# Performance work log

Hardware: AMD Instinct MI355X
Metric: run time of the kernel (lower is better)

Reference implementation:

```python
import jax, jax.numpy as jnp
import numpy as np

HIDDEN = 1024
K_ALIVE = 9          # CodebookConfig.initial_size; alive_mask[:9] = True in __init__
MAX_SIZE = 64
INIT_SCALE = 0.02
DENSITY = 0.05       # SynaptogenesisConfig.initial_density
TAU = 0.07
LN_EPS = 1e-5
NORM_EPS = 1e-12     # F.normalize default eps


def setup_inputs() -> dict:
    key = jax.random.key(0)
    k_h, k_w, k_m, k_p = jax.random.split(key, 4)
    h = jax.random.normal(k_h, (8, 4096, HIDDEN), dtype=jnp.float32)
    weight = jax.random.normal(k_w, (HIDDEN, HIDDEN), dtype=jnp.float32) * 0.02
    mask = (jax.random.uniform(k_m, (HIDDEN, HIDDEN)) < DENSITY).astype(jnp.float32)
    prototypes = jax.random.normal(k_p, (MAX_SIZE, HIDDEN), dtype=jnp.float32) * INIT_SCALE
    gamma = jnp.ones((HIDDEN,), dtype=jnp.float32)   # LayerNorm weight
    beta = jnp.zeros((HIDDEN,), dtype=jnp.float32)   # LayerNorm bias
    return {"h": h, "weight": weight, "mask": mask, "gamma": gamma,
            "beta": beta, "prototypes": prototypes}


def _l2norm(x):
    n = jnp.linalg.norm(x, axis=-1, keepdims=True)
    return x / jnp.maximum(n, NORM_EPS)


def reference(h, weight, mask, gamma, beta, prototypes):
    # SparseSynapticLayer: F.linear(h, weight * mask)  [B,S,D] @ [D,D]^T
    z = jnp.einsum('bsd,od->bso', h, weight * mask)
    # LayerNorm over last dim
    mu = jnp.mean(z, axis=-1, keepdims=True)
    var = jnp.mean(jnp.square(z - mu), axis=-1, keepdims=True)
    z = (z - mu) * jax.lax.rsqrt(var + LN_EPS) * gamma + beta
    # DynamicActionCodebook: cosine similarity to alive prototypes / tau
    live = prototypes[:K_ALIVE]            # alive_mask = first K_ALIVE slots
    logits = jnp.einsum('bsd,kd->bsk', _l2norm(z), _l2norm(live)) / TAU
    return logits, z
```

## Files before the change

### kernel.cpp

```cpp
#include <hip/hip_runtime.h>
#include <stdint.h>

#define HIDDEN 1024
#define MROWS  32768
#define NPROTO 9
#define ZOFF   (MROWS * NPROTO)

typedef __bf16 bf16x8 __attribute__((ext_vector_type(8)));
typedef float  f32x4  __attribute__((ext_vector_type(4)));

__device__ __forceinline__ unsigned short f2bf(float f) {
    unsigned u = __float_as_uint(f);
    u += 0x7fffu + ((u >> 16) & 1u);
    return (unsigned short)(u >> 16);
}

__global__ void k_conv_h(const float* __restrict__ src, unsigned short* __restrict__ dst, int n8) {
    int i0 = blockIdx.x * blockDim.x + threadIdx.x;
    int stride = gridDim.x * blockDim.x;
    for (int i = i0; i < n8; i += stride) {
        const float4* p = (const float4*)(src + (size_t)i * 8);
        float4 a = p[0], b = p[1];
        union { unsigned short us[8]; uint4 v; } o;
        o.us[0] = f2bf(a.x); o.us[1] = f2bf(a.y); o.us[2] = f2bf(a.z); o.us[3] = f2bf(a.w);
        o.us[4] = f2bf(b.x); o.us[5] = f2bf(b.y); o.us[6] = f2bf(b.z); o.us[7] = f2bf(b.w);
        *(uint4*)(dst + (size_t)i * 8) = o.v;
    }
}

__global__ void k_conv_w(const float* __restrict__ w, const float* __restrict__ m,
                         unsigned short* __restrict__ dst, int n8) {
    int i0 = blockIdx.x * blockDim.x + threadIdx.x;
    int stride = gridDim.x * blockDim.x;
    for (int i = i0; i < n8; i += stride) {
        const float4* pw = (const float4*)(w + (size_t)i * 8);
        const float4* pm = (const float4*)(m + (size_t)i * 8);
        float4 a = pw[0], b = pw[1], c = pm[0], d = pm[1];
        union { unsigned short us[8]; uint4 v; } o;
        o.us[0] = f2bf(a.x * c.x); o.us[1] = f2bf(a.y * c.y);
        o.us[2] = f2bf(a.z * c.z); o.us[3] = f2bf(a.w * c.w);
        o.us[4] = f2bf(b.x * d.x); o.us[5] = f2bf(b.y * d.y);
        o.us[6] = f2bf(b.z * d.z); o.us[7] = f2bf(b.w * d.w);
        *(uint4*)(dst + (size_t)i * 8) = o.v;
    }
}

__global__ void k_proto(const float* __restrict__ proto, float* __restrict__ pn) {
    __shared__ float red[4];
    int t = threadIdx.x, k = blockIdx.x;
    float4 v = *(const float4*)(proto + (size_t)k * HIDDEN + t * 4);
    float ss = v.x * v.x + v.y * v.y + v.z * v.z + v.w * v.w;
    #pragma unroll
    for (int m = 1; m < 64; m <<= 1) ss += __shfl_xor(ss, m);
    if ((t & 63) == 0) red[t >> 6] = ss;
    __syncthreads();
    ss = red[0] + red[1] + red[2] + red[3];
    float inv = 1.0f / fmaxf(sqrtf(ss), 1e-12f);
    float4 o; o.x = v.x * inv; o.y = v.y * inv; o.z = v.z * inv; o.w = v.w * inv;
    *(float4*)(pn + (size_t)k * HIDDEN + t * 4) = o;
}

__global__ __launch_bounds__(256, 2) void k_gemm(const unsigned short* __restrict__ A,
                                                 const unsigned short* __restrict__ B,
                                                 float* __restrict__ C) {
    __shared__ unsigned short As[2][128 * 32];
    __shared__ unsigned short Bs[2][128 * 32];
    const int tid = threadIdx.x;
    const int wid = tid >> 6, lane = tid & 63;
    const int bm0 = (int)(blockIdx.x >> 3) * 128;
    const int bn0 = (int)(blockIdx.x & 7) * 128;
    const int wr = wid >> 1, wc = wid & 1;
    const int fr = lane & 15, kq = lane >> 4;

    f32x4 acc[4][4] = {};

    auto stage = [&](int buf, int k0) {
        #pragma unroll
        for (int is = 0; is < 2; ++is) {
            int c = is * 256 + tid;
            int row = c >> 2, seg = c & 3;
            const unsigned short* ga = A + (size_t)(bm0 + row) * HIDDEN + k0 + seg * 8;
            void* la = (void*)((char*)&As[buf][0] + (size_t)(is * 256 + wid * 64) * 16);
            __builtin_amdgcn_global_load_lds((const __attribute__((address_space(1))) void*)ga,
                                             (__attribute__((address_space(3))) void*)la, 16, 0, 0);
            const unsigned short* gb = B + (size_t)(bn0 + row) * HIDDEN + k0 + seg * 8;
            void* lb = (void*)((char*)&Bs[buf][0] + (size_t)(is * 256 + wid * 64) * 16);
            __builtin_amdgcn_global_load_lds((const __attribute__((address_space(1))) void*)gb,
                                             (__attribute__((address_space(3))) void*)lb, 16, 0, 0);
        }
    };

    auto compute = [&](int buf) {
        bf16x8 av[4], bv[4];
        #pragma unroll
        for (int i = 0; i < 4; i++)
            av[i] = *(const bf16x8*)&As[buf][(wr * 64 + i * 16 + fr) * 32 + kq * 8];
        #pragma unroll
        for (int j = 0; j < 4; j++)
            bv[j] = *(const bf16x8*)&Bs[buf][(wc * 64 + j * 16 + fr) * 32 + kq * 8];
        #pragma unroll
        for (int i = 0; i < 4; i++)
            #pragma unroll
            for (int j = 0; j < 4; j++)
                acc[i][j] = __builtin_amdgcn_mfma_f32_16x16x32_bf16(av[i], bv[j], acc[i][j], 0, 0, 0);
    };

    stage(0, 0);
    __syncthreads();
    int cur = 0;
    for (int t = 1; t < 32; t++) {
        stage(cur ^ 1, t * 32);
        compute(cur);
        __syncthreads();
        cur ^= 1;
    }
    compute(cur);

    #pragma unroll
    for (int i = 0; i < 4; i++) {
        #pragma unroll
        for (int j = 0; j < 4; j++) {
            int col = bn0 + wc * 64 + j * 16 + fr;
            int rowb = bm0 + wr * 64 + i * 16 + kq * 4;
            #pragma unroll
            for (int r = 0; r < 4; r++)
                C[(size_t)(rowb + r) * HIDDEN + col] = acc[i][j][r];
        }
    }
}

__global__ __launch_bounds__(256) void k_ln(float* __restrict__ z, float* __restrict__ logits,
                                            const float* __restrict__ gamma, const float* __restrict__ beta,
                                            const float* __restrict__ pn, int waves_total) {
    __shared__ float sp[NPROTO * HIDDEN];
    const int tid = threadIdx.x, wid = tid >> 6, lane = tid & 63;
    #pragma unroll
    for (int i = 0; i < NPROTO * HIDDEN / 4 / 256; i++) {
        int idx = (i * 256 + tid) * 4;
        *(float4*)&sp[idx] = *(const float4*)&pn[idx];
    }
    __syncthreads();

    float4 g4[4], b4[4];
    #pragma unroll
    for (int c = 0; c < 4; c++) {
        g4[c] = *(const float4*)(gamma + lane * 4 + 256 * c);
        b4[c] = *(const float4*)(beta  + lane * 4 + 256 * c);
    }

    const float inv_n = 1.0f / 1024.0f;
    int gw = blockIdx.x * 4 + wid;
    for (int row = gw; row < MROWS; row += waves_total) {
        float* zr = z + (size_t)row * HIDDEN;
        float4 v[4];
        #pragma unroll
        for (int c = 0; c < 4; c++) v[c] = *(const float4*)(zr + lane * 4 + 256 * c);

        float s = 0.f, sq = 0.f;
        #pragma unroll
        for (int c = 0; c < 4; c++) {
            s  += v[c].x + v[c].y + v[c].z + v[c].w;
            sq += v[c].x * v[c].x + v[c].y * v[c].y + v[c].z * v[c].z + v[c].w * v[c].w;
        }
        #pragma unroll
        for (int m = 1; m < 64; m <<= 1) { s += __shfl_xor(s, m); sq += __shfl_xor(sq, m); }

        float mu  = s * inv_n;
        float var = sq * inv_n - mu * mu;
        float rs  = rsqrtf(var + 1e-5f);

        #pragma unroll
        for (int c = 0; c < 4; c++) {
            v[c].x = (v[c].x - mu) * rs * g4[c].x + b4[c].x;
            v[c].y = (v[c].y - mu) * rs * g4[c].y + b4[c].y;
            v[c].z = (v[c].z - mu) * rs * g4[c].z + b4[c].z;
            v[c].w = (v[c].w - mu) * rs * g4[c].w + b4[c].w;
            *(float4*)(zr + lane * 4 + 256 * c) = v[c];
        }

        float part[10];
        #pragma unroll
        for (int k = 0; k < 10; k++) part[k] = 0.f;
        #pragma unroll
        for (int c = 0; c < 4; c++) {
            part[9] += v[c].x * v[c].x + v[c].y * v[c].y + v[c].z * v[c].z + v[c].w * v[c].w;
            #pragma unroll
            for (int k = 0; k < 9; k++) {
                float4 p = *(const float4*)&sp[k * HIDDEN + lane * 4 + 256 * c];
                part[k] += v[c].x * p.x + v[c].y * p.y + v[c].z * p.z + v[c].w * p.w;
            }
        }
        #pragma unroll
        for (int m = 1; m < 64; m <<= 1) {
            #pragma unroll
            for (int k = 0; k < 10; k++) part[k] += __shfl_xor(part[k], m);
        }
        if (lane == 0) {
            float inv = 1.0f / (fmaxf(sqrtf(part[9]), 1e-12f) * 0.07f);
            #pragma unroll
            for (int k = 0; k < 9; k++) logits[(size_t)row * NPROTO + k] = part[k] * inv;
        }
    }
}

extern "C" void kernel_launch(void* const* d_in, const int* in_sizes, int n_in,
                              void* d_out, int out_size, void* d_ws, size_t ws_size,
                              hipStream_t stream) {
    const float* h     = (const float*)d_in[0];
    const float* w     = (const float*)d_in[1];
    const float* mask  = (const float*)d_in[2];
    const float* gamma = (const float*)d_in[3];
    const float* beta  = (const float*)d_in[4];
    const float* proto = (const float*)d_in[5];
    float* out    = (float*)d_out;
    float* logits = out;
    float* z      = out + (size_t)ZOFF;

    char* ws = (char*)d_ws;
    unsigned short* hb = (unsigned short*)ws;
    unsigned short* wm = (unsigned short*)(ws + 67108864);
    float*          pn = (float*)(ws + 67108864 + 2097152);

    k_conv_h<<<4096, 256, 0, stream>>>(h, hb, MROWS * HIDDEN / 8);
    k_conv_w<<<512, 256, 0, stream>>>(w, mask, wm, HIDDEN * HIDDEN / 8);
    k_proto<<<NPROTO, 256, 0, stream>>>(proto, pn);
    k_gemm<<<2048, 256, 0, stream>>>(hb, wm, z);
    k_ln<<<2048, 256, 0, stream>>>(z, logits, gamma, beta, pn, 2048 * 4);
}
```

Before: 201.5 us.

## Fuse GEMM with LayerNorm and cosine-logit epilogue using full-row tiles

Replaces the separate GEMM and LayerNorm/logits kernels with one kernel. Each 512-thread block computes a 64-row by full 1024-column tile, so the row statistics, normalization, z store and prototype dot products all run in the epilogue from registers and LDS. This removes writing z and reading it back from global memory. In exchange it uses a large LDS footprint (136 KB), and each block restages the whole weight matrix for only 64 rows, which lowers weight reuse and occupancy.

```diff
diff --git a/kernel.cpp b/kernel.cpp
--- a/kernel.cpp
+++ b/kernel.cpp
@@ -5,6 +5,8 @@
 #define MROWS  32768
 #define NPROTO 9
 #define ZOFF   (MROWS * NPROTO)
+#define BM     64
+#define BK     32
 
 typedef __bf16 bf16x8 __attribute__((ext_vector_type(8)));
 typedef float  f32x4  __attribute__((ext_vector_type(4)));
@@ -60,146 +62,189 @@
     *(float4*)(pn + (size_t)k * HIDDEN + t * 4) = o;
 }
 
-__global__ __launch_bounds__(256, 2) void k_gemm(const unsigned short* __restrict__ A,
-                                                 const unsigned short* __restrict__ B,
-                                                 float* __restrict__ C) {
-    __shared__ unsigned short As[2][128 * 32];
-    __shared__ unsigned short Bs[2][128 * 32];
+__global__ __launch_bounds__(512, 2) void k_gemm_ln(const unsigned short* __restrict__ A,
+                                                    const unsigned short* __restrict__ B,
+                                                    const float* __restrict__ gamma,
+                                                    const float* __restrict__ beta,
+                                                    const float* __restrict__ pn,
+                                                    float* __restrict__ z,
+                                                    float* __restrict__ logits) {
+    __shared__ char smem[139264];
     const int tid = threadIdx.x;
     const int wid = tid >> 6, lane = tid & 63;
-    const int bm0 = (int)(blockIdx.x >> 3) * 128;
-    const int bn0 = (int)(blockIdx.x & 7) * 128;
-    const int wr = wid >> 1, wc = wid & 1;
     const int fr = lane & 15, kq = lane >> 4;
-
-    f32x4 acc[4][4] = {};
+    const int bm0 = (int)blockIdx.x * BM;
+
+    f32x4 acc[4][8] = {};
 
     auto stage = [&](int buf, int k0) {
-        #pragma unroll
-        for (int is = 0; is < 2; ++is) {
-            int c = is * 256 + tid;
-            int row = c >> 2, seg = c & 3;
+        if (wid < 4) {
+            int row = tid >> 2, seg = tid & 3;
             const unsigned short* ga = A + (size_t)(bm0 + row) * HIDDEN + k0 + seg * 8;
-            void* la = (void*)((char*)&As[buf][0] + (size_t)(is * 256 + wid * 64) * 16);
+            void* la = (void*)(smem + (buf ? 4096 : 0) + (size_t)wid * 1024);
             __builtin_amdgcn_global_load_lds((const __attribute__((address_space(1))) void*)ga,
                                              (__attribute__((address_space(3))) void*)la, 16, 0, 0);
-            const unsigned short* gb = B + (size_t)(bn0 + row) * HIDDEN + k0 + seg * 8;
-            void* lb = (void*)((char*)&Bs[buf][0] + (size_t)(is * 256 + wid * 64) * 16);
+        }
+        #pragma unroll
+        for (int ir = 0; ir < 8; ir++) {
+            int c = ir * 512 + tid;
+            int row = c >> 2, seg = c & 3;
+            const unsigned short* gb = B + (size_t)row * HIDDEN + k0 + seg * 8;
+            void* lb = (void*)(smem + 8192 + (buf ? 65536 : 0) + (size_t)(ir * 512 + wid * 64) * 16);
             __builtin_amdgcn_global_load_lds((const __attribute__((address_space(1))) void*)gb,
                                              (__attribute__((address_space(3))) void*)lb, 16, 0, 0);
         }
     };
 
     auto compute = [&](int buf) {
-        bf16x8 av[4], bv[4];
+        const unsigned short* as = (const unsigned short*)(smem + (buf ? 4096 : 0));
+        const unsigned short* bs = (const unsigned short*)(smem + 8192 + (buf ? 65536 : 0));
+        bf16x8 av[4], bv[8];
         #pragma unroll
         for (int i = 0; i < 4; i++)
-            av[i] = *(const bf16x8*)&As[buf][(wr * 64 + i * 16 + fr) * 32 + kq * 8];
-        #pragma unroll
-        for (int j = 0; j < 4; j++)
-            bv[j] = *(const bf16x8*)&Bs[buf][(wc * 64 + j * 16 + fr) * 32 + kq * 8];
+            av[i] = *(const bf16x8*)&as[(i * 16 + fr) * BK + kq * 8];
+        #pragma unroll
+        for (int j = 0; j < 8; j++)
+            bv[j] = *(const bf16x8*)&bs[(wid * 128 + j * 16 + fr) * BK + kq * 8];
         #pragma unroll
         for (int i = 0; i < 4; i++)
             #pragma unroll
-            for (int j = 0; j < 4; j++)
+            for (int j = 0; j < 8; j++)
                 acc[i][j] = __builtin_amdgcn_mfma_f32_16x16x32_bf16(av[i], bv[j], acc[i][j], 0, 0, 0);
     };
 
     stage(0, 0);
     __syncthreads();
     int cur = 0;
-    for (int t = 1; t < 32; t++) {
-        stage(cur ^ 1, t * 32);
+    for (int t = 1; t < HIDDEN / BK; t++) {
+        stage(cur ^ 1, t * BK);
         compute(cur);
         __syncthreads();
         cur ^= 1;
     }
     compute(cur);
+    __syncthreads();
+
+    float* red_s     = (float*)smem;
+    float* red_sq    = (float*)(smem + 2048);
+    float* mu_lds    = (float*)(smem + 4096);
+    float* rs_lds    = (float*)(smem + 4352);
+    float* proto_lds = (float*)(smem + 8192);
+    float* part_lds  = (float*)(smem + 45056);
+
+    #pragma unroll
+    for (int i2 = 0; i2 < 5; i2++) {
+        int idx = i2 * 512 + tid;
+        if (idx < NPROTO * HIDDEN / 4) ((float4*)proto_lds)[idx] = ((const float4*)pn)[idx];
+    }
 
     #pragma unroll
     for (int i = 0; i < 4; i++) {
         #pragma unroll
-        for (int j = 0; j < 4; j++) {
-            int col = bn0 + wc * 64 + j * 16 + fr;
-            int rowb = bm0 + wr * 64 + i * 16 + kq * 4;
-            #pragma unroll
-            for (int r = 0; r < 4; r++)
-                C[(size_t)(rowb + r) * HIDDEN + col] = acc[i][j][r];
-        }
-    }
-}
-
-__global__ __launch_bounds__(256) void k_ln(float* __restrict__ z, float* __restrict__ logits,
-                                            const float* __restrict__ gamma, const float* __restrict__ beta,
-                                            const float* __restrict__ pn, int waves_total) {
-    __shared__ float sp[NPROTO * HIDDEN];
-    const int tid = threadIdx.x, wid = tid >> 6, lane = tid & 63;
-    #pragma unroll
-    for (int i = 0; i < NPROTO * HIDDEN / 4 / 256; i++) {
-        int idx = (i * 256 + tid) * 4;
-        *(float4*)&sp[idx] = *(const float4*)&pn[idx];
-    }
-    __syncthreads();
-
-    float4 g4[4], b4[4];
-    #pragma unroll
-    for (int c = 0; c < 4; c++) {
-        g4[c] = *(const float4*)(gamma + lane * 4 + 256 * c);
-        b4[c] = *(const float4*)(beta  + lane * 4 + 256 * c);
-    }
-
-    const float inv_n = 1.0f / 1024.0f;
-    int gw = blockIdx.x * 4 + wid;
-    for (int row = gw; row < MROWS; row += waves_total) {
-        float* zr = z + (size_t)row * HIDDEN;
-        float4 v[4];
-        #pragma unroll
-        for (int c = 0; c < 4; c++) v[c] = *(const float4*)(zr + lane * 4 + 256 * c);
-
+        for (int r = 0; r < 4; r++) {
+            float s = 0.f, sq = 0.f;
+            #pragma unroll
+            for (int j = 0; j < 8; j++) { float v = acc[i][j][r]; s += v; sq += v * v; }
+            #pragma unroll
+            for (int m = 1; m < 16; m <<= 1) { s += __shfl_xor(s, m); sq += __shfl_xor(sq, m); }
+            if (fr == 0) {
+                int row = i * 16 + kq * 4 + r;
+                red_s[wid * 64 + row] = s;
+                red_sq[wid * 64 + row] = sq;
+            }
+        }
+    }
+    __syncthreads();
+
+    if (tid < 64) {
         float s = 0.f, sq = 0.f;
         #pragma unroll
-        for (int c = 0; c < 4; c++) {
-            s  += v[c].x + v[c].y + v[c].z + v[c].w;
-            sq += v[c].x * v[c].x + v[c].y * v[c].y + v[c].z * v[c].z + v[c].w * v[c].w;
-        }
-        #pragma unroll
-        for (int m = 1; m < 64; m <<= 1) { s += __shfl_xor(s, m); sq += __shfl_xor(sq, m); }
-
-        float mu  = s * inv_n;
-        float var = sq * inv_n - mu * mu;
-        float rs  = rsqrtf(var + 1e-5f);
-
-        #pragma unroll
-        for (int c = 0; c < 4; c++) {
-            v[c].x = (v[c].x - mu) * rs * g4[c].x + b4[c].x;
-            v[c].y = (v[c].y - mu) * rs * g4[c].y + b4[c].y;
-            v[c].z = (v[c].z - mu) * rs * g4[c].z + b4[c].z;
-            v[c].w = (v[c].w - mu) * rs * g4[c].w + b4[c].w;
-            *(float4*)(zr + lane * 4 + 256 * c) = v[c];
-        }
-
-        float part[10];
-        #pragma unroll
-        for (int k = 0; k < 10; k++) part[k] = 0.f;
-        #pragma unroll
-        for (int c = 0; c < 4; c++) {
-            part[9] += v[c].x * v[c].x + v[c].y * v[c].y + v[c].z * v[c].z + v[c].w * v[c].w;
-            #pragma unroll
-            for (int k = 0; k < 9; k++) {
-                float4 p = *(const float4*)&sp[k * HIDDEN + lane * 4 + 256 * c];
-                part[k] += v[c].x * p.x + v[c].y * p.y + v[c].z * p.z + v[c].w * p.w;
-            }
-        }
-        #pragma unroll
-        for (int m = 1; m < 64; m <<= 1) {
-            #pragma unroll
-            for (int k = 0; k < 10; k++) part[k] += __shfl_xor(part[k], m);
-        }
-        if (lane == 0) {
-            float inv = 1.0f / (fmaxf(sqrtf(part[9]), 1e-12f) * 0.07f);
-            #pragma unroll
-            for (int k = 0; k < 9; k++) logits[(size_t)row * NPROTO + k] = part[k] * inv;
-        }
+        for (int w = 0; w < 8; w++) { s += red_s[w * 64 + tid]; sq += red_sq[w * 64 + tid]; }
+        float mu = s * (1.0f / 1024.0f);
+        float var = sq * (1.0f / 1024.0f) - mu * mu;
+        mu_lds[tid] = mu;
+        rs_lds[tid] = rsqrtf(var + 1e-5f);
+    }
+    __syncthreads();
+
+    float g[8], b[8];
+    #pragma unroll
+    for (int j = 0; j < 8; j++) {
+        int col = wid * 128 + j * 16 + fr;
+        g[j] = gamma[col];
+        b[j] = beta[col];
+    }
+
+    #pragma unroll
+    for (int i = 0; i < 4; i++) {
+        #pragma unroll
+        for (int r = 0; r < 4; r++) {
+            int row = i * 16 + kq * 4 + r;
+            float mu = mu_lds[row], rs = rs_lds[row];
+            float* zr = z + (size_t)(bm0 + row) * HIDDEN + wid * 128;
+            #pragma unroll
+            for (int j = 0; j < 8; j++) {
+                float v = (acc[i][j][r] - mu) * rs * g[j] + b[j];
+                acc[i][j][r] = v;
+                zr[j * 16 + fr] = v;
+            }
+        }
+    }
+
+    #pragma unroll
+    for (int i = 0; i < 4; i++) {
+        #pragma unroll
+        for (int r = 0; r < 4; r++) {
+            float ss = 0.f;
+            #pragma unroll
+            for (int j = 0; j < 8; j++) { float v = acc[i][j][r]; ss += v * v; }
+            #pragma unroll
+            for (int m = 1; m < 16; m <<= 1) ss += __shfl_xor(ss, m);
+            if (fr == 0) {
+                int row = i * 16 + kq * 4 + r;
+                part_lds[(row * 8 + wid) * 10 + 9] = ss;
+            }
+        }
+    }
+    for (int k = 0; k < NPROTO; k++) {
+        float p[8];
+        #pragma unroll
+        for (int j = 0; j < 8; j++) p[j] = proto_lds[k * HIDDEN + wid * 128 + j * 16 + fr];
+        #pragma unroll
+        for (int i = 0; i < 4; i++) {
+            #pragma unroll
+            for (int r = 0; r < 4; r++) {
+                float d = 0.f;
+                #pragma unroll
+                for (int j = 0; j < 8; j++) d += acc[i][j][r] * p[j];
+                #pragma unroll
+                for (int m = 1; m < 16; m <<= 1) d += __shfl_xor(d, m);
+                if (fr == 0) {
+                    int row = i * 16 + kq * 4 + r;
+                    part_lds[(row * 8 + wid) * 10 + k] = d;
+                }
+            }
+        }
+    }
+    __syncthreads();
+
+    if (tid < 64) {
+        int row = tid;
+        float dot[NPROTO];
+        #pragma unroll
+        for (int k = 0; k < NPROTO; k++) dot[k] = 0.f;
+        float ss = 0.f;
+        #pragma unroll
+        for (int w = 0; w < 8; w++) {
+            const float* pl = &part_lds[(row * 8 + w) * 10];
+            #pragma unroll
+            for (int k = 0; k < NPROTO; k++) dot[k] += pl[k];
+            ss += pl[9];
+        }
+        float inv = 1.0f / (fmaxf(sqrtf(ss), 1e-12f) * 0.07f);
+        float* lr = logits + (size_t)(bm0 + row) * NPROTO;
+        #pragma unroll
+        for (int k = 0; k < NPROTO; k++) lr[k] = dot[k] * inv;
     }
 }
 
@@ -224,6 +269,5 @@
     k_conv_h<<<4096, 256, 0, stream>>>(h, hb, MROWS * HIDDEN / 8);
     k_conv_w<<<512, 256, 0, stream>>>(w, mask, wm, HIDDEN * HIDDEN / 8);
     k_proto<<<NPROTO, 256, 0, stream>>>(proto, pn);
-    k_gemm<<<2048, 256, 0, stream>>>(hb, wm, z);
-    k_ln<<<2048, 256, 0, stream>>>(z, logits, gamma, beta, pn, 2048 * 4);
-}
+    k_gemm_ln<<<MROWS / BM, 512, 0, stream>>>(hb, wm, gamma, beta, pn, z, logits);
+}
```

Result: slower. 226.7 us (+12.5%).

## Fuse fp32-to-bf16 conversion of h into GEMM and store bf16 pre-norm output

Applied to the files above, without the earlier changes.

Drops the separate h conversion kernel. The GEMM now loads fp32 h directly into registers and converts to bf16 while writing to LDS, overlapping this with the MFMA compute. The GEMM writes the pre-LayerNorm result as bf16 to workspace instead of fp32 into the output, which halves that intermediate's write and read traffic. Block indices are also remapped so each XCD gets a contiguous set of M rows for L2 reuse. In exchange, A-tile loading now goes through registers, and rounding the pre-norm activations to bf16 adds precision loss.

```diff
diff --git a/kernel.cpp b/kernel.cpp
--- a/kernel.cpp
+++ b/kernel.cpp
@@ -14,18 +14,8 @@
     u += 0x7fffu + ((u >> 16) & 1u);
     return (unsigned short)(u >> 16);
 }
-
-__global__ void k_conv_h(const float* __restrict__ src, unsigned short* __restrict__ dst, int n8) {
-    int i0 = blockIdx.x * blockDim.x + threadIdx.x;
-    int stride = gridDim.x * blockDim.x;
-    for (int i = i0; i < n8; i += stride) {
-        const float4* p = (const float4*)(src + (size_t)i * 8);
-        float4 a = p[0], b = p[1];
-        union { unsigned short us[8]; uint4 v; } o;
-        o.us[0] = f2bf(a.x); o.us[1] = f2bf(a.y); o.us[2] = f2bf(a.z); o.us[3] = f2bf(a.w);
-        o.us[4] = f2bf(b.x); o.us[5] = f2bf(b.y); o.us[6] = f2bf(b.z); o.us[7] = f2bf(b.w);
-        *(uint4*)(dst + (size_t)i * 8) = o.v;
-    }
+__device__ __forceinline__ float bf2f(unsigned short u) {
+    return __uint_as_float(((unsigned)u) << 16);
 }
 
 __global__ void k_conv_w(const float* __restrict__ w, const float* __restrict__ m,
@@ -60,36 +50,52 @@
     *(float4*)(pn + (size_t)k * HIDDEN + t * 4) = o;
 }
 
-__global__ __launch_bounds__(256, 2) void k_gemm(const unsigned short* __restrict__ A,
+__global__ __launch_bounds__(256, 2) void k_gemm(const float* __restrict__ H,
                                                  const unsigned short* __restrict__ B,
-                                                 float* __restrict__ C) {
+                                                 unsigned short* __restrict__ ZP) {
     __shared__ unsigned short As[2][128 * 32];
     __shared__ unsigned short Bs[2][128 * 32];
     const int tid = threadIdx.x;
     const int wid = tid >> 6, lane = tid & 63;
-    const int bm0 = (int)(blockIdx.x >> 3) * 128;
-    const int bn0 = (int)(blockIdx.x & 7) * 128;
+    const int hw = (int)blockIdx.x;
+    const int xcd = hw & 7, nblk = (hw >> 3) & 7, mloc = hw >> 6;
+    const int bm0 = (xcd * 32 + mloc) * 128;
+    const int bn0 = nblk * 128;
     const int wr = wid >> 1, wc = wid & 1;
     const int fr = lane & 15, kq = lane >> 4;
 
+    const int arow = tid >> 1, ahalf = tid & 1;
+    const float* ha = H + (size_t)(bm0 + arow) * HIDDEN + ahalf * 16;
+
     f32x4 acc[4][4] = {};
 
-    auto stage = [&](int buf, int k0) {
+    auto loadA = [&](float4* f, int k0) {
+        const float4* p = (const float4*)(ha + k0);
+        #pragma unroll
+        for (int q = 0; q < 4; q++) f[q] = p[q];
+    };
+    auto writeA = [&](int buf, const float4* f) {
+        union { unsigned short us[16]; uint4 v[2]; } o;
+        #pragma unroll
+        for (int q = 0; q < 4; q++) {
+            o.us[q * 4 + 0] = f2bf(f[q].x); o.us[q * 4 + 1] = f2bf(f[q].y);
+            o.us[q * 4 + 2] = f2bf(f[q].z); o.us[q * 4 + 3] = f2bf(f[q].w);
+        }
+        uint4* dst = (uint4*)&As[buf][arow * 32 + ahalf * 16];
+        dst[0] = o.v[0];
+        dst[1] = o.v[1];
+    };
+    auto stageB = [&](int buf, int k0) {
         #pragma unroll
         for (int is = 0; is < 2; ++is) {
             int c = is * 256 + tid;
             int row = c >> 2, seg = c & 3;
-            const unsigned short* ga = A + (size_t)(bm0 + row) * HIDDEN + k0 + seg * 8;
-            void* la = (void*)((char*)&As[buf][0] + (size_t)(is * 256 + wid * 64) * 16);
-            __builtin_amdgcn_global_load_lds((const __attribute__((address_space(1))) void*)ga,
-                                             (__attribute__((address_space(3))) void*)la, 16, 0, 0);
             const unsigned short* gb = B + (size_t)(bn0 + row) * HIDDEN + k0 + seg * 8;
             void* lb = (void*)((char*)&Bs[buf][0] + (size_t)(is * 256 + wid * 64) * 16);
             __builtin_amdgcn_global_load_lds((const __attribute__((address_space(1))) void*)gb,
                                              (__attribute__((address_space(3))) void*)lb, 16, 0, 0);
         }
     };
-
     auto compute = [&](int buf) {
         bf16x8 av[4], bv[4];
         #pragma unroll
@@ -105,12 +111,18 @@
                 acc[i][j] = __builtin_amdgcn_mfma_f32_16x16x32_bf16(av[i], bv[j], acc[i][j], 0, 0, 0);
     };
 
-    stage(0, 0);
+    float4 af[4];
+    loadA(af, 0);
+    stageB(0, 0);
+    writeA(0, af);
     __syncthreads();
     int cur = 0;
     for (int t = 1; t < 32; t++) {
-        stage(cur ^ 1, t * 32);
+        float4 an[4];
+        loadA(an, t * 32);
+        stageB(cur ^ 1, t * 32);
         compute(cur);
+        writeA(cur ^ 1, an);
         __syncthreads();
         cur ^= 1;
     }
@@ -124,12 +136,13 @@
             int rowb = bm0 + wr * 64 + i * 16 + kq * 4;
             #pragma unroll
             for (int r = 0; r < 4; r++)
-                C[(size_t)(rowb + r) * HIDDEN + col] = acc[i][j][r];
-        }
-    }
-}
-
-__global__ __launch_bounds__(256) void k_ln(float* __restrict__ z, float* __restrict__ logits,
+                ZP[(size_t)(rowb + r) * HIDDEN + col] = f2bf(acc[i][j][r]);
+        }
+    }
+}
+
+__global__ __launch_bounds__(256) void k_ln(const unsigned short* __restrict__ zp,
+                                            float* __restrict__ z, float* __restrict__ logits,
                                             const float* __restrict__ gamma, const float* __restrict__ beta,
                                             const float* __restrict__ pn, int waves_total) {
     __shared__ float sp[NPROTO * HIDDEN];
@@ -151,10 +164,13 @@
     const float inv_n = 1.0f / 1024.0f;
     int gw = blockIdx.x * 4 + wid;
     for (int row = gw; row < MROWS; row += waves_total) {
-        float* zr = z + (size_t)row * HIDDEN;
+        const unsigned short* zr = zp + (size_t)row * HIDDEN;
         float4 v[4];
         #pragma unroll
-        for (int c = 0; c < 4; c++) v[c] = *(const float4*)(zr + lane * 4 + 256 * c);
+        for (int c = 0; c < 4; c++) {
+            ushort4 u = *(const ushort4*)(zr + lane * 4 + 256 * c);
+            v[c].x = bf2f(u.x); v[c].y = bf2f(u.y); v[c].z = bf2f(u.z); v[c].w = bf2f(u.w);
+        }
 
         float s = 0.f, sq = 0.f;
         #pragma unroll
@@ -169,13 +185,14 @@
         float var = sq * inv_n - mu * mu;
         float rs  = rsqrtf(var + 1e-5f);
 
+        float* zo = z + (size_t)row * HIDDEN;
         #pragma unroll
         for (int c = 0; c < 4; c++) {
             v[c].x = (v[c].x - mu) * rs * g4[c].x + b4[c].x;
             v[c].y = (v[c].y - mu) * rs * g4[c].y + b4[c].y;
             v[c].z = (v[c].z - mu) * rs * g4[c].z + b4[c].z;
             v[c].w = (v[c].w - mu) * rs * g4[c].w + b4[c].w;
-            *(float4*)(zr + lane * 4 + 256 * c) = v[c];
+            *(float4*)(zo + lane * 4 + 256 * c) = v[c];
         }
 
         float part[10];
@@ -217,13 +234,12 @@
     float* z      = out + (size_t)ZOFF;
 
     char* ws = (char*)d_ws;
-    unsigned short* hb = (unsigned short*)ws;
+    unsigned short* zp = (unsigned short*)ws;
     unsigned short* wm = (unsigned short*)(ws + 67108864);
     float*          pn = (float*)(ws + 67108864 + 2097152);
 
-    k_conv_h<<<4096, 256, 0, stream>>>(h, hb, MROWS * HIDDEN / 8);
     k_conv_w<<<512, 256, 0, stream>>>(w, mask, wm, HIDDEN * HIDDEN / 8);
     k_proto<<<NPROTO, 256, 0, stream>>>(proto, pn);
-    k_gemm<<<2048, 256, 0, stream>>>(hb, wm, z);
-    k_ln<<<2048, 256, 0, stream>>>(z, logits, gamma, beta, pn, 2048 * 4);
-}
+    k_gemm<<<2048, 256, 0, stream>>>(h, wm, zp);
+    k_ln<<<2048, 256, 0, stream>>>(zp, z, logits, gamma, beta, pn, 2048 * 4);
+}
```

Measured after the change: 201.7 us. Within noise of the previous version (+0.1%).
